# Kernel tuning notes

Measured on AMD Instinct MI355X. Metric: run time of the kernel, lower is better.

## Reference

```python
import jax, jax.numpy as jnp
import numpy as np

TAU = 0.5

def setup_inputs() -> dict:
    key = jax.random.key(0)
    ks = jax.random.split(key, 6)
    B, L, D, P = 4, 4096, 256, 256
    return {
        "X1": jax.random.normal(ks[0], (B, L, D), dtype=jnp.float32),
        "X2": jax.random.normal(ks[1], (B, L, D), dtype=jnp.float32),
        "W1": jax.random.normal(ks[2], (P, D), dtype=jnp.float32) * (1.0 / np.sqrt(D)),
        "b1": jax.random.normal(ks[3], (P,), dtype=jnp.float32) * 0.01,
        "W2": jax.random.normal(ks[4], (D, P), dtype=jnp.float32) * (1.0 / np.sqrt(P)),
        "b2": jax.random.normal(ks[5], (D,), dtype=jnp.float32) * 0.01,
    }

def _projection(z, W1, b1, W2, b2):
    h = jax.nn.elu(z @ W1.T + b1)
    return h @ W2.T + b2

def _normalize(z, eps=1e-12):
    n = jnp.linalg.norm(z, axis=-1, keepdims=True)
    return z / jnp.maximum(n, eps)

def _semi_loss(z1, z2, tau):
    # z1, z2: [B, L, D]
    z1n = _normalize(z1)
    z2n = _normalize(z2)
    refl = jnp.exp(jnp.einsum('bld,bmd->blm', z1n, z1n) / tau)   # [B, L, L]
    between = jnp.exp(jnp.einsum('bld,bmd->blm', z1n, z2n) / tau)
    refl_diag = jnp.diagonal(refl, axis1=-2, axis2=-1)           # [B, L]
    between_diag = jnp.diagonal(between, axis1=-2, axis2=-1)
    denom = refl.sum(axis=-1) + between.sum(axis=-1) - refl_diag
    return -jnp.log(between_diag / denom).sum(axis=-1)           # [B]

def reference(X1, X2, W1, b1, W2, b2):
    h1 = _projection(X1, W1, b1, W2, b2)
    h2 = _projection(X2, W1, b1, W2, b2)
    l1 = _semi_loss(h1, h2, TAU)
    l2 = _semi_loss(h2, h1, TAU)
    return ((l1 + l2) * 0.5).mean()
```

## Files before the change

kernel.cpp:

```cpp
#include <hip/hip_runtime.h>
#include <math.h>


typedef __attribute__((ext_vector_type(8))) short short8;
typedef __attribute__((ext_vector_type(4))) short short4v;
typedef __attribute__((ext_vector_type(4))) float float4v;
typedef __attribute__((ext_vector_type(8))) int int8v;
typedef __attribute__((ext_vector_type(4))) int int4v;

#if defined(__has_builtin)
#if __has_builtin(__builtin_amdgcn_exp2f)
#define EXP2F(x) __builtin_amdgcn_exp2f(x)
#endif
#endif
#ifndef EXP2F
#define EXP2F(x) __expf(0.69314718056f * (x))
#endif

__device__ __forceinline__ short f2bf(float f) {
    unsigned u = __builtin_bit_cast(unsigned, f);
    u += 0x7fffu + ((u >> 16) & 1u);
    return (short)(u >> 16);
}

__device__ __forceinline__ unsigned char f2fp8(float f) {
    float af = fabsf(f);
    unsigned s = (__builtin_bit_cast(unsigned, f) >> 31) << 7;
    if (af < 0.015625f) {
        int q = (int)rintf(af * 512.0f);
        return (unsigned char)(s | (unsigned)q);
    }
    unsigned au = __builtin_bit_cast(unsigned, af);
    au += 0x7FFFFu + ((au >> 20) & 1u);
    int e = (int)(au >> 23) - 127;
    unsigned m = (au >> 20) & 7u;
    return (unsigned char)(s | (unsigned)((e + 7) << 3) | m);
}

__device__ __forceinline__ void gl_lds16(const void* g, void* l) {
    __builtin_amdgcn_global_load_lds(
        (const __attribute__((address_space(1))) void*)g,
        (__attribute__((address_space(3))) void*)l, 16, 0, 0);
}

__global__ __launch_bounds__(256) void convW_zero_kernel(
    const float* __restrict__ W1, const float* __restrict__ W2,
    short* __restrict__ d1, short* __restrict__ d2,
    float* __restrict__ S, float* __restrict__ out)
{
    int i = blockIdx.x * 256 + threadIdx.x;
    const float* src = (i < 16384) ? W1 : W2;
    short* dst = (i < 16384) ? d1 : d2;
    int j = i & 16383;
    float4v v = ((const float4v*)src)[j];
    short4v o;
    o.x = f2bf(v.x); o.y = f2bf(v.y); o.z = f2bf(v.z); o.w = f2bf(v.w);
    ((short4v*)dst)[j] = o;
    S[i] = 0.f;
    if (i == 0) *out = 0.f;
}

__global__ __launch_bounds__(256, 2) void fusedproj_kernel(
    const float* __restrict__ X1, const float* __restrict__ X2,
    const short* __restrict__ W1bf, const float* __restrict__ b1,
    const short* __restrict__ W2bf, const float* __restrict__ b2,
    unsigned char* __restrict__ zn8)
{
    __shared__ short lsB[16384];
    __shared__ short lsH[16384];
    __shared__ float rssq[4][64];
    __shared__ float rinv[64];

    const int arow0 = blockIdx.x * 64;
    const int tid  = threadIdx.x;
    const int w    = tid >> 6;
    const int lane = tid & 63;
    const int quad = lane >> 4;
    const int l15  = lane & 15;

    const int set = arow0 >> 14;
    const float* Xs = (set ? X2 : X1) + (size_t)(arow0 & 16383) * 256;

    float4v acc[4][4];
#pragma unroll
    for (int mi = 0; mi < 4; ++mi)
#pragma unroll
        for (int ni = 0; ni < 4; ++ni)
            acc[mi][ni] = (float4v){0.f, 0.f, 0.f, 0.f};

    for (int kt = 0; kt < 4; ++kt) {
        const int kbase = kt * 64;
#pragma unroll
        for (int r = 0; r < 8; ++r) {
            const int c   = w * 8 + r;
            const int s   = c * 64 + lane;
            const int kc  = s >> 8;
            const int row = s & 255;
            gl_lds16(W1bf + (size_t)row * 256 + kbase + kc * 8,
                     lsB + (size_t)c * 512);
        }
        __syncthreads();
#pragma unroll
        for (int ks = 0; ks < 2; ++ks) {
            const int kc = ks * 4 + quad;
            short8 af[4], bfv[4];
#pragma unroll
            for (int mi = 0; mi < 4; ++mi) {
                const float* xp = Xs + (size_t)(mi * 16 + l15) * 256
                                  + kbase + kc * 8;
                float4v a0 = *(const float4v*)xp;
                float4v a1 = *(const float4v*)(xp + 4);
                short8 t;
                t[0] = f2bf(a0.x); t[1] = f2bf(a0.y);
                t[2] = f2bf(a0.z); t[3] = f2bf(a0.w);
                t[4] = f2bf(a1.x); t[5] = f2bf(a1.y);
                t[6] = f2bf(a1.z); t[7] = f2bf(a1.w);
                af[mi] = t;
            }
#pragma unroll
            for (int ni = 0; ni < 4; ++ni)
                bfv[ni] = *(const short8*)(lsB +
                    ((size_t)kc * 256 + w * 64 + ni * 16 + l15) * 8);
#pragma unroll
            for (int mi = 0; mi < 4; ++mi)
#pragma unroll
                for (int ni = 0; ni < 4; ++ni)
                    acc[mi][ni] = __builtin_amdgcn_mfma_f32_16x16x32_bf16(
                        af[mi], bfv[ni], acc[mi][ni], 0, 0, 0);
        }
        __syncthreads();
    }

    {
        const int rowbase = quad * 4;
        const int colbase = w * 64 + l15;
#pragma unroll
        for (int ni = 0; ni < 4; ++ni) {
            const int p  = colbase + ni * 16;
            const float bv = b1[p];
#pragma unroll
            for (int mi = 0; mi < 4; ++mi)
#pragma unroll
                for (int reg = 0; reg < 4; ++reg) {
                    const int row = rowbase + mi * 16 + reg;
                    float v = acc[mi][ni][reg] + bv;
                    v = (v > 0.f) ? v : expm1f(v);
                    lsH[(size_t)(p >> 3) * 512 + row * 8 + (p & 7)] = f2bf(v);
                }
        }
    }

#pragma unroll
    for (int mi = 0; mi < 4; ++mi)
#pragma unroll
        for (int ni = 0; ni < 4; ++ni)
            acc[mi][ni] = (float4v){0.f, 0.f, 0.f, 0.f};

    for (int kt = 0; kt < 4; ++kt) {
        const int kbase = kt * 64;
#pragma unroll
        for (int r = 0; r < 8; ++r) {
            const int c   = w * 8 + r;
            const int s   = c * 64 + lane;
            const int kc  = s >> 8;
            const int row = s & 255;
            gl_lds16(W2bf + (size_t)row * 256 + kbase + kc * 8,
                     lsB + (size_t)c * 512);
        }
        __syncthreads();
#pragma unroll
        for (int ks = 0; ks < 2; ++ks) {
            const int kc = ks * 4 + quad;
            short8 af[4], bfv[4];
#pragma unroll
            for (int mi = 0; mi < 4; ++mi)
                af[mi] = *(const short8*)(lsH +
                    ((size_t)(kt * 8 + kc) * 64 + mi * 16 + l15) * 8);
#pragma unroll
            for (int ni = 0; ni < 4; ++ni)
                bfv[ni] = *(const short8*)(lsB +
                    ((size_t)kc * 256 + w * 64 + ni * 16 + l15) * 8);
#pragma unroll
            for (int mi = 0; mi < 4; ++mi)
#pragma unroll
                for (int ni = 0; ni < 4; ++ni)
                    acc[mi][ni] = __builtin_amdgcn_mfma_f32_16x16x32_bf16(
                        af[mi], bfv[ni], acc[mi][ni], 0, 0, 0);
        }
        __syncthreads();
    }

#pragma unroll
    for (int ni = 0; ni < 4; ++ni) {
        const float bv = b2[w * 64 + ni * 16 + l15];
#pragma unroll
        for (int mi = 0; mi < 4; ++mi)
#pragma unroll
            for (int reg = 0; reg < 4; ++reg)
                acc[mi][ni][reg] += bv;
    }
    float ps[4][4];
#pragma unroll
    for (int mi = 0; mi < 4; ++mi)
#pragma unroll
        for (int reg = 0; reg < 4; ++reg) {
            float s = 0.f;
#pragma unroll
            for (int ni = 0; ni < 4; ++ni) {
                float v = acc[mi][ni][reg];
                s += v * v;
            }
            s += __shfl_xor(s, 1); s += __shfl_xor(s, 2);
            s += __shfl_xor(s, 4); s += __shfl_xor(s, 8);
            ps[mi][reg] = s;
        }
    if (l15 == 0) {
#pragma unroll
        for (int mi = 0; mi < 4; ++mi)
#pragma unroll
            for (int reg = 0; reg < 4; ++reg)
                rssq[w][mi * 16 + quad * 4 + reg] = ps[mi][reg];
    }
    __syncthreads();
    if (tid < 64) {
        float ssq = rssq[0][tid] + rssq[1][tid] + rssq[2][tid] + rssq[3][tid];
        rinv[tid] = 1.69864360f / fmaxf(sqrtf(ssq), 1e-12f);
    }
    __syncthreads();

    const int r0  = arow0;
    const int bb  = (r0 >> 12) & 3;
    const int l0  = r0 & 4095;
    unsigned char* dst = zn8 + ((size_t)(bb * 2 + set) * 4096 + l0) * 256;
    const int colbase = w * 64 + l15;
#pragma unroll
    for (int mi = 0; mi < 4; ++mi)
#pragma unroll
        for (int reg = 0; reg < 4; ++reg) {
            const int rl = mi * 16 + quad * 4 + reg;
            const float inv = rinv[rl];
#pragma unroll
            for (int ni = 0; ni < 4; ++ni)
                dst[(size_t)rl * 256 + colbase + ni * 16] =
                    f2fp8(acc[mi][ni][reg] * inv);
        }
}

#if defined(__has_builtin)
#if __has_builtin(__builtin_amdgcn_mfma_scale_f32_16x16x128_f8f6f4)
#define HAVE_MX 1
#endif
#endif

__global__ __launch_bounds__(256, 2) void gram_fp8_sym_kernel(
    const unsigned char* __restrict__ zn8, float* __restrict__ S,
    float* __restrict__ Cc, float* __restrict__ out)
{
    const int bx    = blockIdx.x;
    const int xcd   = bx & 7;
    const int batch = xcd >> 1;
    const int sub   = (bx >> 3) * 2 + (xcd & 1);
    const int p     = sub >> 2;
    const int qu    = sub & 3;
    const int u0    = (qu == 0) ? 0 : 17 + (qu - 1) * 16;
    const int u1    = u0 + ((qu == 0) ? 17 : 16);
    const int ubrk  = 64 - p;

    const unsigned char* Z = zn8 + (size_t)batch * 2097152;

    const int tid  = threadIdx.x;
    const int w    = tid >> 6;
    const int lane = tid & 63;
    const int wm   = w & 1;
    const int wn   = w >> 1;
    const int quad = lane >> 4;
    const int l15  = lane & 15;

#define TJ_OF(u)  ((u) < ubrk ? p + (u) : (u) - 1)
#define ROW_OF(u) ((u) < ubrk ? p : 63 - p)

    float rs[4][4];
#pragma unroll
    for (int mi = 0; mi < 4; ++mi)
#pragma unroll
        for (int reg = 0; reg < 4; ++reg)
            rs[mi][reg] = 0.f;
    float dsum = 0.f;

#define FLUSH_RS(rowstripe)                                                   \
    {                                                                         \
        float* Sr = S + (size_t)batch * 8192 + (rowstripe) * 128 + wm * 64;   \
        _Pragma("unroll")                                                     \
        for (int mi = 0; mi < 4; ++mi)                                        \
            _Pragma("unroll")                                                 \
            for (int reg = 0; reg < 4; ++reg) {                               \
                float v = rs[mi][reg];                                        \
                v += __shfl_xor(v, 1); v += __shfl_xor(v, 2);                 \
                v += __shfl_xor(v, 4); v += __shfl_xor(v, 8);                 \
                if (l15 == 0)                                                 \
                    atomicAdd(&Sr[mi * 16 + quad * 4 + reg], v);              \
                rs[mi][reg] = 0.f;                                            \
            }                                                                 \
    }

    int currow = ROW_OF(u0);

#ifdef HAVE_MX
    int8v afr[4][2];
#define LOAD_A(rowstripe)                                                     \
    {                                                                         \
        const unsigned char* Ab = Z + (size_t)((rowstripe) * 128 + wm * 64) * 256; \
        _Pragma("unroll")                                                     \
        for (int mi = 0; mi < 4; ++mi)                                        \
            _Pragma("unroll")                                                 \
            for (int ks = 0; ks < 2; ++ks) {                                  \
                const unsigned char* pA = Ab + (size_t)(mi * 16 + l15) * 256  \
                                          + ks * 128 + quad * 32;             \
                int4v lo = *(const int4v*)pA;                                 \
                int4v hi = *(const int4v*)(pA + 16);                          \
                afr[mi][ks] = __builtin_shufflevector(lo, hi, 0,1,2,3,4,5,6,7); \
            }                                                                 \
    }
#else
    long afr[4][8];
#define LOAD_A(rowstripe)                                                     \
    {                                                                         \
        const unsigned char* Ab = Z + (size_t)((rowstripe) * 128 + wm * 64) * 256; \
        _Pragma("unroll")                                                     \
        for (int mi = 0; mi < 4; ++mi)                                        \
            _Pragma("unroll")                                                 \
            for (int kc = 0; kc < 8; ++kc)                                    \
                afr[mi][kc] = *(const long*)(Ab + (size_t)(mi * 16 + l15) * 256 \
                                             + kc * 32 + quad * 8);           \
    }
#endif

    LOAD_A(currow);

    for (int ui = u0; ui < u1; ++ui) {
        const int row = ROW_OF(ui);
        const int tj  = TJ_OF(ui);
        if (row != currow) {
            FLUSH_RS(currow);
            LOAD_A(row);
            currow = row;
        }

        const unsigned char* Bb = Z + ((size_t)tj * 128 + wn * 64) * 256;

        float4v acc[4][4];
#pragma unroll
        for (int mi = 0; mi < 4; ++mi)
#pragma unroll
            for (int ni = 0; ni < 4; ++ni)
                acc[mi][ni] = (float4v){0.f, 0.f, 0.f, 0.f};

#ifdef HAVE_MX
        int8v bfv[2][4];
#pragma unroll
        for (int ks = 0; ks < 2; ++ks)
#pragma unroll
            for (int ni = 0; ni < 4; ++ni) {
                const unsigned char* pB = Bb + (size_t)(ni * 16 + l15) * 256
                                          + ks * 128 + quad * 32;
                int4v lo = *(const int4v*)pB;
                int4v hi = *(const int4v*)(pB + 16);
                bfv[ks][ni] = __builtin_shufflevector(lo, hi, 0,1,2,3,4,5,6,7);
            }
        __builtin_amdgcn_s_setprio(1);
#pragma unroll
        for (int ks = 0; ks < 2; ++ks)
#pragma unroll
            for (int mi = 0; mi < 4; ++mi)
#pragma unroll
                for (int ni = 0; ni < 4; ++ni)
                    acc[mi][ni] = __builtin_amdgcn_mfma_scale_f32_16x16x128_f8f6f4(
                        afr[mi][ks], bfv[ks][ni], acc[mi][ni],
                        0, 0,
                        0, 0x7F7F7F7F,
                        0, 0x7F7F7F7F);
        __builtin_amdgcn_s_setprio(0);
#else
#pragma unroll
        for (int kc = 0; kc < 8; ++kc) {
            long bfv[4];
#pragma unroll
            for (int ni = 0; ni < 4; ++ni)
                bfv[ni] = *(const long*)(Bb + (size_t)(ni * 16 + l15) * 256
                                         + kc * 32 + quad * 8);
#pragma unroll
            for (int mi = 0; mi < 4; ++mi)
#pragma unroll
                for (int ni = 0; ni < 4; ++ni)
                    acc[mi][ni] = __builtin_amdgcn_mfma_f32_16x16x32_fp8_fp8(
                        afr[mi][kc], bfv[ni], acc[mi][ni], 0, 0, 0);
        }
#endif

        if (tj == row + 32) {
#pragma unroll
            for (int mi = 0; mi < 4; ++mi)
#pragma unroll
                for (int ni = 0; ni < 4; ++ni)
#pragma unroll
                    for (int reg = 0; reg < 4; ++reg) {
                        const int r = wm * 64 + mi * 16 + quad * 4 + reg;
                        const int c = wn * 64 + ni * 16 + l15;
                        if (r == c) dsum += acc[mi][ni][reg];
                    }
        }

#pragma unroll
        for (int mi = 0; mi < 4; ++mi)
#pragma unroll
            for (int ni = 0; ni < 4; ++ni)
#pragma unroll
                for (int reg = 0; reg < 4; ++reg)
                    acc[mi][ni][reg] = EXP2F(acc[mi][ni][reg]);

#pragma unroll
        for (int mi = 0; mi < 4; ++mi)
#pragma unroll
            for (int reg = 0; reg < 4; ++reg)
                rs[mi][reg] += acc[mi][0][reg] + acc[mi][1][reg]
                             + acc[mi][2][reg] + acc[mi][3][reg];

        if (tj > row) {
            float* Cd = Cc + ((size_t)batch * 128 + row * 2 + wm) * 8192
                        + tj * 128 + wn * 64;
#pragma unroll
            for (int ni = 0; ni < 4; ++ni) {
                float s = 0.f;
#pragma unroll
                for (int mi = 0; mi < 4; ++mi)
#pragma unroll
                    for (int reg = 0; reg < 4; ++reg)
                        s += acc[mi][ni][reg];
                s += __shfl_xor(s, 16); s += __shfl_xor(s, 32);
                if (quad == 0)
                    Cd[ni * 16 + l15] = s;
            }
        }
    }

    FLUSH_RS(currow);

    {
        float dv = dsum;
        dv += __shfl_xor(dv, 1);  dv += __shfl_xor(dv, 2);
        dv += __shfl_xor(dv, 4);  dv += __shfl_xor(dv, 8);
        dv += __shfl_xor(dv, 16); dv += __shfl_xor(dv, 32);
        if (lane == 0 && dv != 0.f)
            atomicAdd(out, -0.17328680f * dv);
    }
#undef LOAD_A
#undef FLUSH_RS
#undef TJ_OF
#undef ROW_OF
}

__global__ __launch_bounds__(256) void final_log_kernel(
    const float* __restrict__ S, const float* __restrict__ Cc,
    float* __restrict__ out)
{
    __shared__ float red[4];
    const int tid  = threadIdx.x;
    const int w    = tid >> 6;
    const int lane = tid & 63;
    const float E2 = 7.3890560989306495f;

    const int i = blockIdx.x * 256 + tid;
    const int b = i >> 13;
    const int q = i & 8191;
    float s = S[i];
    const float* Cp = Cc + (size_t)b * 128 * 8192 + q;
    const int np = (q >> 7) * 2;
    for (int r = 0; r < np; ++r)
        s += Cp[(size_t)r * 8192];
    float acc = logf(s - E2);

    acc += __shfl_xor(acc, 1);  acc += __shfl_xor(acc, 2);
    acc += __shfl_xor(acc, 4);  acc += __shfl_xor(acc, 8);
    acc += __shfl_xor(acc, 16); acc += __shfl_xor(acc, 32);
    if (lane == 0) red[w] = acc;
    __syncthreads();
    if (tid == 0)
        atomicAdd(out, 0.125f * (red[0] + red[1] + red[2] + red[3]));
}

extern "C" void kernel_launch(void* const* d_in, const int* in_sizes, int n_in,
                              void* d_out, int out_size, void* d_ws, size_t ws_size,
                              hipStream_t stream)
{
    const float* X1 = (const float*)d_in[0];
    const float* X2 = (const float*)d_in[1];
    const float* W1 = (const float*)d_in[2];
    const float* b1 = (const float*)d_in[3];
    const float* W2 = (const float*)d_in[4];
    const float* b2 = (const float*)d_in[5];

    char* ws = (char*)d_ws;
    float* S    = (float*)(ws + 0);
    short* W1bf = (short*)(ws + 131072);
    short* W2bf = (short*)(ws + 262144);
    unsigned char* zn8 = (unsigned char*)(ws + 393216);
    float* Cc   = (float*)(ws + 8781824);

    convW_zero_kernel<<<128, 256, 0, stream>>>(W1, W2, W1bf, W2bf,
                                               S, (float*)d_out);
    fusedproj_kernel<<<512, 256, 0, stream>>>(X1, X2, W1bf, b1, W2bf, b2, zn8);
    gram_fp8_sym_kernel<<<512, 256, 0, stream>>>(zn8, S, Cc, (float*)d_out);
    final_log_kernel<<<128, 256, 0, stream>>>(S, Cc, (float*)d_out);
}
```

Before: 223.0 us.

## Use 8-wave blocks and double-buffered LDS staging of Gram B tiles

Both the projection and the FP8 Gram kernels now run 512-thread blocks with 8 waves, halving each wave's output tile. In the Gram kernel, B tiles are no longer read straight from global memory by every wave. They are staged into a double-buffered LDS area with global-to-LDS loads, so the next tile is prefetched while the current one is multiplied, and each staged tile is shared by the waves. The column-sum partial buffer grows to four row-groups per stripe, so the final log kernel reads twice as many partials. The cost is a block-wide barrier per tile, more LDS per block, and a larger workspace footprint.

```diff
diff --git a/kernel.cpp b/kernel.cpp
--- a/kernel.cpp
+++ b/kernel.cpp
@@ -60,7 +60,7 @@
     if (i == 0) *out = 0.f;
 }
 
-__global__ __launch_bounds__(256, 2) void fusedproj_kernel(
+__global__ __launch_bounds__(512, 4) void fusedproj_kernel(
     const float* __restrict__ X1, const float* __restrict__ X2,
     const short* __restrict__ W1bf, const float* __restrict__ b1,
     const short* __restrict__ W2bf, const float* __restrict__ b2,
@@ -68,7 +68,7 @@
 {
     __shared__ short lsB[16384];
     __shared__ short lsH[16384];
-    __shared__ float rssq[4][64];
+    __shared__ float rssq[8][64];
     __shared__ float rinv[64];
 
     const int arow0 = blockIdx.x * 64;
@@ -81,18 +81,18 @@
     const int set = arow0 >> 14;
     const float* Xs = (set ? X2 : X1) + (size_t)(arow0 & 16383) * 256;
 
-    float4v acc[4][4];
+    float4v acc[4][2];
 #pragma unroll
     for (int mi = 0; mi < 4; ++mi)
 #pragma unroll
-        for (int ni = 0; ni < 4; ++ni)
+        for (int ni = 0; ni < 2; ++ni)
             acc[mi][ni] = (float4v){0.f, 0.f, 0.f, 0.f};
 
     for (int kt = 0; kt < 4; ++kt) {
         const int kbase = kt * 64;
 #pragma unroll
-        for (int r = 0; r < 8; ++r) {
-            const int c   = w * 8 + r;
+        for (int r = 0; r < 4; ++r) {
+            const int c   = w * 4 + r;
             const int s   = c * 64 + lane;
             const int kc  = s >> 8;
             const int row = s & 255;
@@ -103,7 +103,7 @@
 #pragma unroll
         for (int ks = 0; ks < 2; ++ks) {
             const int kc = ks * 4 + quad;
-            short8 af[4], bfv[4];
+            short8 af[4], bfv[2];
 #pragma unroll
             for (int mi = 0; mi < 4; ++mi) {
                 const float* xp = Xs + (size_t)(mi * 16 + l15) * 256
@@ -118,13 +118,13 @@
                 af[mi] = t;
             }
 #pragma unroll
-            for (int ni = 0; ni < 4; ++ni)
+            for (int ni = 0; ni < 2; ++ni)
                 bfv[ni] = *(const short8*)(lsB +
-                    ((size_t)kc * 256 + w * 64 + ni * 16 + l15) * 8);
+                    ((size_t)kc * 256 + w * 32 + ni * 16 + l15) * 8);
 #pragma unroll
             for (int mi = 0; mi < 4; ++mi)
 #pragma unroll
-                for (int ni = 0; ni < 4; ++ni)
+                for (int ni = 0; ni < 2; ++ni)
                     acc[mi][ni] = __builtin_amdgcn_mfma_f32_16x16x32_bf16(
                         af[mi], bfv[ni], acc[mi][ni], 0, 0, 0);
         }
@@ -132,20 +132,18 @@
     }
 
     {
-        const int rowbase = quad * 4;
-        const int colbase = w * 64 + l15;
-#pragma unroll
-        for (int ni = 0; ni < 4; ++ni) {
-            const int p  = colbase + ni * 16;
-            const float bv = b1[p];
+#pragma unroll
+        for (int ni = 0; ni < 2; ++ni) {
+            const int pcol = w * 32 + ni * 16 + l15;
+            const float bv = b1[pcol];
 #pragma unroll
             for (int mi = 0; mi < 4; ++mi)
 #pragma unroll
                 for (int reg = 0; reg < 4; ++reg) {
-                    const int row = rowbase + mi * 16 + reg;
+                    const int row = mi * 16 + quad * 4 + reg;
                     float v = acc[mi][ni][reg] + bv;
                     v = (v > 0.f) ? v : expm1f(v);
-                    lsH[(size_t)(p >> 3) * 512 + row * 8 + (p & 7)] = f2bf(v);
+                    lsH[(size_t)(pcol >> 3) * 512 + row * 8 + (pcol & 7)] = f2bf(v);
                 }
         }
     }
@@ -153,14 +151,14 @@
 #pragma unroll
     for (int mi = 0; mi < 4; ++mi)
 #pragma unroll
-        for (int ni = 0; ni < 4; ++ni)
+        for (int ni = 0; ni < 2; ++ni)
             acc[mi][ni] = (float4v){0.f, 0.f, 0.f, 0.f};
 
     for (int kt = 0; kt < 4; ++kt) {
         const int kbase = kt * 64;
 #pragma unroll
-        for (int r = 0; r < 8; ++r) {
-            const int c   = w * 8 + r;
+        for (int r = 0; r < 4; ++r) {
+            const int c   = w * 4 + r;
             const int s   = c * 64 + lane;
             const int kc  = s >> 8;
             const int row = s & 255;
@@ -171,19 +169,19 @@
 #pragma unroll
         for (int ks = 0; ks < 2; ++ks) {
             const int kc = ks * 4 + quad;
-            short8 af[4], bfv[4];
+            short8 af[4], bfv[2];
 #pragma unroll
             for (int mi = 0; mi < 4; ++mi)
                 af[mi] = *(const short8*)(lsH +
                     ((size_t)(kt * 8 + kc) * 64 + mi * 16 + l15) * 8);
 #pragma unroll
-            for (int ni = 0; ni < 4; ++ni)
+            for (int ni = 0; ni < 2; ++ni)
                 bfv[ni] = *(const short8*)(lsB +
-                    ((size_t)kc * 256 + w * 64 + ni * 16 + l15) * 8);
+                    ((size_t)kc * 256 + w * 32 + ni * 16 + l15) * 8);
 #pragma unroll
             for (int mi = 0; mi < 4; ++mi)
 #pragma unroll
-                for (int ni = 0; ni < 4; ++ni)
+                for (int ni = 0; ni < 2; ++ni)
                     acc[mi][ni] = __builtin_amdgcn_mfma_f32_16x16x32_bf16(
                         af[mi], bfv[ni], acc[mi][ni], 0, 0, 0);
         }
@@ -191,8 +189,8 @@
     }
 
 #pragma unroll
-    for (int ni = 0; ni < 4; ++ni) {
-        const float bv = b2[w * 64 + ni * 16 + l15];
+    for (int ni = 0; ni < 2; ++ni) {
+        const float bv = b2[w * 32 + ni * 16 + l15];
 #pragma unroll
         for (int mi = 0; mi < 4; ++mi)
 #pragma unroll
@@ -206,7 +204,7 @@
         for (int reg = 0; reg < 4; ++reg) {
             float s = 0.f;
 #pragma unroll
-            for (int ni = 0; ni < 4; ++ni) {
+            for (int ni = 0; ni < 2; ++ni) {
                 float v = acc[mi][ni][reg];
                 s += v * v;
             }
@@ -223,7 +221,9 @@
     }
     __syncthreads();
     if (tid < 64) {
-        float ssq = rssq[0][tid] + rssq[1][tid] + rssq[2][tid] + rssq[3][tid];
+        float ssq = 0.f;
+#pragma unroll
+        for (int j = 0; j < 8; ++j) ssq += rssq[j][tid];
         rinv[tid] = 1.69864360f / fmaxf(sqrtf(ssq), 1e-12f);
     }
     __syncthreads();
@@ -232,7 +232,6 @@
     const int bb  = (r0 >> 12) & 3;
     const int l0  = r0 & 4095;
     unsigned char* dst = zn8 + ((size_t)(bb * 2 + set) * 4096 + l0) * 256;
-    const int colbase = w * 64 + l15;
 #pragma unroll
     for (int mi = 0; mi < 4; ++mi)
 #pragma unroll
@@ -240,8 +239,8 @@
             const int rl = mi * 16 + quad * 4 + reg;
             const float inv = rinv[rl];
 #pragma unroll
-            for (int ni = 0; ni < 4; ++ni)
-                dst[(size_t)rl * 256 + colbase + ni * 16] =
+            for (int ni = 0; ni < 2; ++ni)
+                dst[(size_t)rl * 256 + w * 32 + ni * 16 + l15] =
                     f2fp8(acc[mi][ni][reg] * inv);
         }
 }
@@ -252,10 +251,12 @@
 #endif
 #endif
 
-__global__ __launch_bounds__(256, 2) void gram_fp8_sym_kernel(
+__global__ __launch_bounds__(512, 4) void gram_fp8_sym_kernel(
     const unsigned char* __restrict__ zn8, float* __restrict__ S,
     float* __restrict__ Cc, float* __restrict__ out)
 {
+    __shared__ unsigned char lsB[2][32768];
+
     const int bx    = blockIdx.x;
     const int xcd   = bx & 7;
     const int batch = xcd >> 1;
@@ -271,17 +272,31 @@
     const int tid  = threadIdx.x;
     const int w    = tid >> 6;
     const int lane = tid & 63;
-    const int wm   = w & 1;
-    const int wn   = w >> 1;
+    const int wm   = w & 3;
+    const int wn   = w >> 2;
     const int quad = lane >> 4;
     const int l15  = lane & 15;
 
 #define TJ_OF(u)  ((u) < ubrk ? p + (u) : (u) - 1)
 #define ROW_OF(u) ((u) < ubrk ? p : 63 - p)
 
-    float rs[4][4];
-#pragma unroll
-    for (int mi = 0; mi < 4; ++mi)
+#define STAGE_B(t, buf)                                                       \
+    {                                                                         \
+        const unsigned char* Bb = Z + (size_t)(t) * 128 * 256;                \
+        _Pragma("unroll")                                                     \
+        for (int r = 0; r < 4; ++r) {                                         \
+            const int c   = w * 4 + r;                                        \
+            const int u_  = c * 64 + lane;                                    \
+            const int kp  = u_ >> 7;                                          \
+            const int col = u_ & 127;                                         \
+            gl_lds16(Bb + (size_t)col * 256 + kp * 16,                        \
+                     &lsB[buf][(size_t)c * 1024]);                            \
+        }                                                                     \
+    }
+
+    float rs[2][4];
+#pragma unroll
+    for (int mi = 0; mi < 2; ++mi)
 #pragma unroll
         for (int reg = 0; reg < 4; ++reg)
             rs[mi][reg] = 0.f;
@@ -289,9 +304,9 @@
 
 #define FLUSH_RS(rowstripe)                                                   \
     {                                                                         \
-        float* Sr = S + (size_t)batch * 8192 + (rowstripe) * 128 + wm * 64;   \
+        float* Sr = S + (size_t)batch * 8192 + (rowstripe) * 128 + wm * 32;   \
         _Pragma("unroll")                                                     \
-        for (int mi = 0; mi < 4; ++mi)                                        \
+        for (int mi = 0; mi < 2; ++mi)                                        \
             _Pragma("unroll")                                                 \
             for (int reg = 0; reg < 4; ++reg) {                               \
                 float v = rs[mi][reg];                                        \
@@ -306,12 +321,12 @@
     int currow = ROW_OF(u0);
 
 #ifdef HAVE_MX
-    int8v afr[4][2];
+    int8v afr[2][2];
 #define LOAD_A(rowstripe)                                                     \
     {                                                                         \
-        const unsigned char* Ab = Z + (size_t)((rowstripe) * 128 + wm * 64) * 256; \
+        const unsigned char* Ab = Z + (size_t)((rowstripe) * 128 + wm * 32) * 256; \
         _Pragma("unroll")                                                     \
-        for (int mi = 0; mi < 4; ++mi)                                        \
+        for (int mi = 0; mi < 2; ++mi)                                        \
             _Pragma("unroll")                                                 \
             for (int ks = 0; ks < 2; ++ks) {                                  \
                 const unsigned char* pA = Ab + (size_t)(mi * 16 + l15) * 256  \
@@ -322,12 +337,12 @@
             }                                                                 \
     }
 #else
-    long afr[4][8];
+    long afr[2][8];
 #define LOAD_A(rowstripe)                                                     \
     {                                                                         \
-        const unsigned char* Ab = Z + (size_t)((rowstripe) * 128 + wm * 64) * 256; \
+        const unsigned char* Ab = Z + (size_t)((rowstripe) * 128 + wm * 32) * 256; \
         _Pragma("unroll")                                                     \
-        for (int mi = 0; mi < 4; ++mi)                                        \
+        for (int mi = 0; mi < 2; ++mi)                                        \
             _Pragma("unroll")                                                 \
             for (int kc = 0; kc < 8; ++kc)                                    \
                 afr[mi][kc] = *(const long*)(Ab + (size_t)(mi * 16 + l15) * 256 \
@@ -336,8 +351,11 @@
 #endif
 
     LOAD_A(currow);
+    STAGE_B(TJ_OF(u0), 0);
+    __syncthreads();
 
     for (int ui = u0; ui < u1; ++ui) {
+        const int buf = (ui - u0) & 1;
         const int row = ROW_OF(ui);
         const int tj  = TJ_OF(ui);
         if (row != currow) {
@@ -345,73 +363,76 @@
             LOAD_A(row);
             currow = row;
         }
-
-        const unsigned char* Bb = Z + ((size_t)tj * 128 + wn * 64) * 256;
-
-        float4v acc[4][4];
-#pragma unroll
-        for (int mi = 0; mi < 4; ++mi)
+        if (ui + 1 < u1) STAGE_B(TJ_OF(ui + 1), buf ^ 1);
+
+        float4v acc[2][4];
+#pragma unroll
+        for (int mi = 0; mi < 2; ++mi)
 #pragma unroll
             for (int ni = 0; ni < 4; ++ni)
                 acc[mi][ni] = (float4v){0.f, 0.f, 0.f, 0.f};
 
+        const unsigned char* lb = &lsB[buf][0];
+        __builtin_amdgcn_s_setprio(1);
 #ifdef HAVE_MX
-        int8v bfv[2][4];
-#pragma unroll
-        for (int ks = 0; ks < 2; ++ks)
+#pragma unroll
+        for (int ks = 0; ks < 2; ++ks) {
+            const int kp0 = ks * 8 + quad * 2;
+            int8v bfv[4];
 #pragma unroll
             for (int ni = 0; ni < 4; ++ni) {
-                const unsigned char* pB = Bb + (size_t)(ni * 16 + l15) * 256
-                                          + ks * 128 + quad * 32;
+                const unsigned char* pB = lb +
+                    ((size_t)kp0 * 128 + wn * 64 + ni * 16 + l15) * 16;
                 int4v lo = *(const int4v*)pB;
-                int4v hi = *(const int4v*)(pB + 16);
-                bfv[ks][ni] = __builtin_shufflevector(lo, hi, 0,1,2,3,4,5,6,7);
+                int4v hi = *(const int4v*)(pB + 2048);
+                bfv[ni] = __builtin_shufflevector(lo, hi, 0,1,2,3,4,5,6,7);
             }
-        __builtin_amdgcn_s_setprio(1);
-#pragma unroll
-        for (int ks = 0; ks < 2; ++ks)
-#pragma unroll
-            for (int mi = 0; mi < 4; ++mi)
+#pragma unroll
+            for (int mi = 0; mi < 2; ++mi)
 #pragma unroll
                 for (int ni = 0; ni < 4; ++ni)
                     acc[mi][ni] = __builtin_amdgcn_mfma_scale_f32_16x16x128_f8f6f4(
-                        afr[mi][ks], bfv[ks][ni], acc[mi][ni],
+                        afr[mi][ks], bfv[ni], acc[mi][ni],
                         0, 0,
                         0, 0x7F7F7F7F,
                         0, 0x7F7F7F7F);
-        __builtin_amdgcn_s_setprio(0);
+        }
 #else
 #pragma unroll
         for (int kc = 0; kc < 8; ++kc) {
+            const int kseg = kc * 4 + quad;
+            const int kp   = kseg >> 1;
+            const int hf   = kseg & 1;
             long bfv[4];
 #pragma unroll
             for (int ni = 0; ni < 4; ++ni)
-                bfv[ni] = *(const long*)(Bb + (size_t)(ni * 16 + l15) * 256
-                                         + kc * 32 + quad * 8);
-#pragma unroll
-            for (int mi = 0; mi < 4; ++mi)
+                bfv[ni] = *(const long*)(lb +
+                    ((size_t)kp * 128 + wn * 64 + ni * 16 + l15) * 16 + hf * 8);
+#pragma unroll
+            for (int mi = 0; mi < 2; ++mi)
 #pragma unroll
                 for (int ni = 0; ni < 4; ++ni)
                     acc[mi][ni] = __builtin_amdgcn_mfma_f32_16x16x32_fp8_fp8(
                         afr[mi][kc], bfv[ni], acc[mi][ni], 0, 0, 0);
         }
 #endif
+        __builtin_amdgcn_s_setprio(0);
 
         if (tj == row + 32) {
 #pragma unroll
-            for (int mi = 0; mi < 4; ++mi)
+            for (int mi = 0; mi < 2; ++mi)
 #pragma unroll
                 for (int ni = 0; ni < 4; ++ni)
 #pragma unroll
                     for (int reg = 0; reg < 4; ++reg) {
-                        const int r = wm * 64 + mi * 16 + quad * 4 + reg;
+                        const int r = wm * 32 + mi * 16 + quad * 4 + reg;
                         const int c = wn * 64 + ni * 16 + l15;
                         if (r == c) dsum += acc[mi][ni][reg];
                     }
         }
 
 #pragma unroll
-        for (int mi = 0; mi < 4; ++mi)
+        for (int mi = 0; mi < 2; ++mi)
 #pragma unroll
             for (int ni = 0; ni < 4; ++ni)
 #pragma unroll
@@ -419,20 +440,20 @@
                     acc[mi][ni][reg] = EXP2F(acc[mi][ni][reg]);
 
 #pragma unroll
-        for (int mi = 0; mi < 4; ++mi)
+        for (int mi = 0; mi < 2; ++mi)
 #pragma unroll
             for (int reg = 0; reg < 4; ++reg)
                 rs[mi][reg] += acc[mi][0][reg] + acc[mi][1][reg]
                              + acc[mi][2][reg] + acc[mi][3][reg];
 
         if (tj > row) {
-            float* Cd = Cc + ((size_t)batch * 128 + row * 2 + wm) * 8192
+            float* Cd = Cc + ((size_t)batch * 256 + row * 4 + wm) * 8192
                         + tj * 128 + wn * 64;
 #pragma unroll
             for (int ni = 0; ni < 4; ++ni) {
                 float s = 0.f;
 #pragma unroll
-                for (int mi = 0; mi < 4; ++mi)
+                for (int mi = 0; mi < 2; ++mi)
 #pragma unroll
                     for (int reg = 0; reg < 4; ++reg)
                         s += acc[mi][ni][reg];
@@ -441,6 +462,7 @@
                     Cd[ni * 16 + l15] = s;
             }
         }
+        __syncthreads();
     }
 
     FLUSH_RS(currow);
@@ -453,6 +475,7 @@
         if (lane == 0 && dv != 0.f)
             atomicAdd(out, -0.17328680f * dv);
     }
+#undef STAGE_B
 #undef LOAD_A
 #undef FLUSH_RS
 #undef TJ_OF
@@ -473,8 +496,8 @@
     const int b = i >> 13;
     const int q = i & 8191;
     float s = S[i];
-    const float* Cp = Cc + (size_t)b * 128 * 8192 + q;
-    const int np = (q >> 7) * 2;
+    const float* Cp = Cc + (size_t)b * 256 * 8192 + q;
+    const int np = (q >> 7) * 4;
     for (int r = 0; r < np; ++r)
         s += Cp[(size_t)r * 8192];
     float acc = logf(s - E2);
@@ -508,7 +531,7 @@
 
     convW_zero_kernel<<<128, 256, 0, stream>>>(W1, W2, W1bf, W2bf,
                                                S, (float*)d_out);
-    fusedproj_kernel<<<512, 256, 0, stream>>>(X1, X2, W1bf, b1, W2bf, b2, zn8);
-    gram_fp8_sym_kernel<<<512, 256, 0, stream>>>(zn8, S, Cc, (float*)d_out);
+    fusedproj_kernel<<<512, 512, 0, stream>>>(X1, X2, W1bf, b1, W2bf, b2, zn8);
+    gram_fp8_sym_kernel<<<512, 512, 0, stream>>>(zn8, S, Cc, (float*)d_out);
     final_log_kernel<<<128, 256, 0, stream>>>(S, Cc, (float*)d_out);
 }
```

Result: slower. 367.9 us (+65.0%).

## Double-buffer B tiles through LDS with async global-to-LDS staging

Applied to the files above, without the earlier changes.

The symmetric FP8 Gram kernel now stages each 128x256 B tile into a double-buffered LDS array using direct global-to-LDS 16-byte loads, prefetching the next tile while MFMAs run on the current one. B fragments are read from LDS in a k-pair-major layout instead of straight from global memory by each wave. The intent is to share B loads across the waves and hide global latency. In exchange it uses 64 KB of LDS per block, which may limit the two-blocks-per-CU target, and adds a block barrier every iteration.

```diff
diff --git a/kernel.cpp b/kernel.cpp
--- a/kernel.cpp
+++ b/kernel.cpp
@@ -256,6 +256,8 @@
     const unsigned char* __restrict__ zn8, float* __restrict__ S,
     float* __restrict__ Cc, float* __restrict__ out)
 {
+    __shared__ unsigned char lsB[2][32768];
+
     const int bx    = blockIdx.x;
     const int xcd   = bx & 7;
     const int batch = xcd >> 1;
@@ -278,6 +280,20 @@
 
 #define TJ_OF(u)  ((u) < ubrk ? p + (u) : (u) - 1)
 #define ROW_OF(u) ((u) < ubrk ? p : 63 - p)
+
+#define STAGE_B(t, buf)                                                       \
+    {                                                                         \
+        const unsigned char* Bb = Z + (size_t)(t) * 128 * 256;                \
+        _Pragma("unroll")                                                     \
+        for (int r = 0; r < 8; ++r) {                                         \
+            const int c   = w * 8 + r;                                        \
+            const int u_  = c * 64 + lane;                                    \
+            const int kp  = u_ >> 7;                                          \
+            const int col = u_ & 127;                                         \
+            gl_lds16(Bb + (size_t)col * 256 + kp * 16,                        \
+                     &lsB[buf][(size_t)c * 1024]);                            \
+        }                                                                     \
+    }
 
     float rs[4][4];
 #pragma unroll
@@ -336,8 +352,11 @@
 #endif
 
     LOAD_A(currow);
+    STAGE_B(TJ_OF(u0), 0);
+    __syncthreads();
 
     for (int ui = u0; ui < u1; ++ui) {
+        const int buf = (ui - u0) & 1;
         const int row = ROW_OF(ui);
         const int tj  = TJ_OF(ui);
         if (row != currow) {
@@ -345,8 +364,7 @@
             LOAD_A(row);
             currow = row;
         }
-
-        const unsigned char* Bb = Z + ((size_t)tj * 128 + wn * 64) * 256;
+        if (ui + 1 < u1) STAGE_B(TJ_OF(ui + 1), buf ^ 1);
 
         float4v acc[4][4];
 #pragma unroll
@@ -355,39 +373,42 @@
             for (int ni = 0; ni < 4; ++ni)
                 acc[mi][ni] = (float4v){0.f, 0.f, 0.f, 0.f};
 
+        const unsigned char* lb = &lsB[buf][0];
+        __builtin_amdgcn_s_setprio(1);
 #ifdef HAVE_MX
-        int8v bfv[2][4];
-#pragma unroll
-        for (int ks = 0; ks < 2; ++ks)
+#pragma unroll
+        for (int ks = 0; ks < 2; ++ks) {
+            const int kp0 = ks * 8 + quad * 2;
+            int8v bfv[4];
 #pragma unroll
             for (int ni = 0; ni < 4; ++ni) {
-                const unsigned char* pB = Bb + (size_t)(ni * 16 + l15) * 256
-                                          + ks * 128 + quad * 32;
+                const unsigned char* pB = lb +
+                    ((size_t)kp0 * 128 + wn * 64 + ni * 16 + l15) * 16;
                 int4v lo = *(const int4v*)pB;
-                int4v hi = *(const int4v*)(pB + 16);
-                bfv[ks][ni] = __builtin_shufflevector(lo, hi, 0,1,2,3,4,5,6,7);
+                int4v hi = *(const int4v*)(pB + 2048);
+                bfv[ni] = __builtin_shufflevector(lo, hi, 0,1,2,3,4,5,6,7);
             }
-        __builtin_amdgcn_s_setprio(1);
-#pragma unroll
-        for (int ks = 0; ks < 2; ++ks)
 #pragma unroll
             for (int mi = 0; mi < 4; ++mi)
 #pragma unroll
                 for (int ni = 0; ni < 4; ++ni)
                     acc[mi][ni] = __builtin_amdgcn_mfma_scale_f32_16x16x128_f8f6f4(
-                        afr[mi][ks], bfv[ks][ni], acc[mi][ni],
+                        afr[mi][ks], bfv[ni], acc[mi][ni],
                         0, 0,
                         0, 0x7F7F7F7F,
                         0, 0x7F7F7F7F);
-        __builtin_amdgcn_s_setprio(0);
+        }
 #else
 #pragma unroll
         for (int kc = 0; kc < 8; ++kc) {
+            const int kseg = kc * 4 + quad;
+            const int kp   = kseg >> 1;
+            const int hf   = kseg & 1;
             long bfv[4];
 #pragma unroll
             for (int ni = 0; ni < 4; ++ni)
-                bfv[ni] = *(const long*)(Bb + (size_t)(ni * 16 + l15) * 256
-                                         + kc * 32 + quad * 8);
+                bfv[ni] = *(const long*)(lb +
+                    ((size_t)kp * 128 + wn * 64 + ni * 16 + l15) * 16 + hf * 8);
 #pragma unroll
             for (int mi = 0; mi < 4; ++mi)
 #pragma unroll
@@ -396,6 +417,7 @@
                         afr[mi][kc], bfv[ni], acc[mi][ni], 0, 0, 0);
         }
 #endif
+        __builtin_amdgcn_s_setprio(0);
 
         if (tj == row + 32) {
 #pragma unroll
@@ -441,6 +463,7 @@
                     Cd[ni * 16 + l15] = s;
             }
         }
+        __syncthreads();
     }
 
     FLUSH_RS(currow);
@@ -453,6 +476,7 @@
         if (lane == 0 && dv != 0.f)
             atomicAdd(out, -0.17328680f * dv);
     }
+#undef STAGE_B
 #undef LOAD_A
 #undef FLUSH_RS
 #undef TJ_OF
```

After: 212.5 us. 1.05x faster.
